# Performance work log

Hardware: AMD Instinct MI355X
Metric: run time of the kernel (lower is better)

## Reference

```python
import jax, jax.numpy as jnp
import numpy as np

N, D_IN, D_OUT, E = 8192, 2048, 2048, 8


def setup_inputs() -> dict:
    key = jax.random.key(0)
    k0, k1, k2, k3, k4, k5 = jax.random.split(key, 6)
    s = 1.0 / np.sqrt(D_IN)  # torch nn.Linear default init range
    return {
        "inputs": jax.random.normal(k0, (N, D_IN), jnp.float32),
        "condition": jax.random.normal(k1, (N, D_IN), jnp.float32),
        "Wp": jax.random.uniform(k2, (E, D_IN), jnp.float32, -s, s),
        "bp": jax.random.uniform(k3, (E,), jnp.float32, -s, s),
        "We": jax.random.uniform(k4, (E, D_OUT, D_IN), jnp.float32, -s, s),
        "be": jax.random.uniform(k5, (E, D_OUT), jnp.float32, -s, s),
    }


def reference(inputs, condition, Wp, bp, We, be):
    # predictor: gating logits [N, E]
    prediction = condition @ Wp.T + bp
    # straight-through multiplier: value == 1, gradient flows to prediction
    multiply = jnp.ones_like(prediction) + (prediction - jax.lax.stop_gradient(prediction))
    # run ALL experts on the full batch (faithful to the original): [E, N, F]
    expert_out = jnp.einsum('nd,efd->enf', inputs, We) + be[:, None, :]
    combined = multiply.T[:, :, None] * expert_out  # [E, N, F]
    # select the argmax expert per row
    idx = jnp.argmax(prediction, axis=-1)  # [N]
    result = combined[idx, jnp.arange(prediction.shape[0])]  # [N, F]
    return result
```

## Files before the change

### kernel.cpp

```cpp
#include <hip/hip_runtime.h>
#include <hip/hip_bf16.h>
#include <stdint.h>

#define N_ROWS 8192
#define DIN 2048
#define DOUT 2048
#define NE 8

#define BM 128
#define BN 128
#define BK 64
#define MAX_RT 71

typedef __bf16 bf16x8 __attribute__((ext_vector_type(8)));
typedef float f32x4 __attribute__((ext_vector_type(4)));

__device__ __forceinline__ uint32_t f2bf(float f) {
  uint32_t u = __builtin_bit_cast(uint32_t, f);
  uint32_t r = u + 0x7FFFu + ((u >> 16) & 1u);
  return r >> 16;
}

__device__ __forceinline__ void gl2lds16(const void* g, void* l) {
  __builtin_amdgcn_global_load_lds(
      (const __attribute__((address_space(1))) unsigned int*)g,
      (__attribute__((address_space(3))) unsigned int*)l, 16, 0, 0);
}

__global__ __launch_bounds__(256) void gate_kernel(
    const float* __restrict__ cond, const float* __restrict__ Wp,
    const float* __restrict__ bp, int* __restrict__ idx)
{
  const int lane = threadIdx.x & 63;
  const int wid  = threadIdx.x >> 6;
  const int row  = blockIdx.x * 4 + wid;

  double acc[NE];
  #pragma unroll
  for (int e = 0; e < NE; ++e) acc[e] = 0.0;

  const float4* crow = (const float4*)(cond + (size_t)row * DIN);
  const float4* wp4  = (const float4*)Wp;
  #pragma unroll
  for (int i = 0; i < DIN / 256; ++i) {
    float4 c = crow[i * 64 + lane];
    #pragma unroll
    for (int e = 0; e < NE; ++e) {
      float4 w = wp4[e * (DIN / 4) + i * 64 + lane];
      acc[e] += (double)c.x * w.x + (double)c.y * w.y
              + (double)c.z * w.z + (double)c.w * w.w;
    }
  }
  #pragma unroll
  for (int e = 0; e < NE; ++e) {
    double v = acc[e];
    #pragma unroll
    for (int off = 32; off > 0; off >>= 1) v += __shfl_down(v, off, 64);
    acc[e] = v;
  }
  if (lane == 0) {
    int best = 0; double bv = acc[0] + (double)bp[0];
    #pragma unroll
    for (int e = 1; e < NE; ++e) {
      double v = acc[e] + (double)bp[e];
      if (v > bv) { bv = v; best = e; }
    }
    idx[row] = best;
  }
}

__global__ __launch_bounds__(256) void hist_kernel(
    const int* __restrict__ idx, int* __restrict__ counts)
{
  __shared__ int lc[NE];
  const int t = threadIdx.x;
  if (t < NE) lc[t] = 0;
  __syncthreads();
  int n = blockIdx.x * 256 + t;
  atomicAdd(&lc[idx[n]], 1);
  __syncthreads();
  if (t < NE && lc[t] > 0) atomicAdd(&counts[t], lc[t]);
}

__global__ void scan_kernel(const int* __restrict__ counts, int* __restrict__ offsets) {
  if (threadIdx.x == 0 && blockIdx.x == 0) {
    int s = 0;
    for (int e = 0; e < NE; ++e) { offsets[e] = s; s += counts[e]; }
  }
}

__global__ __launch_bounds__(256) void scatter_kernel(
    const int* __restrict__ idx, const int* __restrict__ offsets,
    int* __restrict__ fill, int* __restrict__ rows)
{
  __shared__ int lc[NE], lb[NE];
  const int t = threadIdx.x;
  if (t < NE) lc[t] = 0;
  __syncthreads();
  int n = blockIdx.x * 256 + t;
  int e = idx[n];
  int my = atomicAdd(&lc[e], 1);
  __syncthreads();
  if (t < NE) lb[t] = (lc[t] > 0) ? atomicAdd(&fill[t], lc[t]) : 0;
  __syncthreads();
  rows[offsets[e] + lb[e] + my] = n;
}

__global__ __launch_bounds__(256) void conv_kernel(
    const float* __restrict__ src, __hip_bfloat16* __restrict__ dst, size_t nchunks)
{
  const size_t stride = (size_t)gridDim.x * 256;
  for (size_t c = (size_t)blockIdx.x * 256 + threadIdx.x; c < nchunks; c += stride) {
    float4 v0 = ((const float4*)src)[c * 2];
    float4 v1 = ((const float4*)src)[c * 2 + 1];
    uint4 o;
    o.x = f2bf(v0.x) | (f2bf(v0.y) << 16);
    o.y = f2bf(v0.z) | (f2bf(v0.w) << 16);
    o.z = f2bf(v1.x) | (f2bf(v1.y) << 16);
    o.w = f2bf(v1.z) | (f2bf(v1.w) << 16);
    ((uint4*)dst)[c] = o;
  }
}

__global__ __launch_bounds__(256) void moe_gemm3(
    const __hip_bfloat16* __restrict__ Xb, const __hip_bfloat16* __restrict__ Web,
    const float* __restrict__ be, const int* __restrict__ counts,
    const int* __restrict__ offsets, const int* __restrict__ rows,
    float* __restrict__ out)
{
  __shared__ __align__(16) __hip_bfloat16 As[2][BM * BK];
  __shared__ __align__(16) __hip_bfloat16 Bs[2][BN * BK];
  __shared__ int rowid[BM];

  const int ct = blockIdx.x;
  const int rt = blockIdx.y;

  int e = 0, racc = 0, cnt = 0;
  for (; e < NE; ++e) {
    cnt = counts[e];
    int tiles = (cnt + BM - 1) / BM;
    if (rt < racc + tiles) break;
    racc += tiles;
  }
  if (e == NE) return;
  const int row0 = (rt - racc) * BM;
  const int base = offsets[e];
  const int t = threadIdx.x;

  if (t < BM)
    rowid[t] = (row0 + t < cnt) ? rows[base + row0 + t] : -1;
  __syncthreads();

  const __hip_bfloat16* aSrcP[4];
  #pragma unroll
  for (int p = 0; p < 4; ++p) {
    int c = p * 256 + t;
    int gr = rowid[c >> 3];
    if (gr < 0) gr = 0;
    aSrcP[p] = Xb + (size_t)gr * DIN + (c & 7) * 8;
  }
  const size_t bcol0 = (size_t)e * DOUT + (size_t)ct * BN;
  const __hip_bfloat16* bSrc0 = Web + (bcol0 + (t >> 3)) * DIN + (t & 7) * 8;

  const int lane = t & 63;
  const int wv   = t >> 6;
  const int wr   = wv >> 1, wc = wv & 1;
  const int g    = lane >> 4, fr = lane & 15;

  f32x4 acc[4][4];
  #pragma unroll
  for (int m = 0; m < 4; ++m)
    #pragma unroll
    for (int n = 0; n < 4; ++n)
      acc[m][n] = 0.0f;

#define STAGE(buf, k0) do {                                                     \
    _Pragma("unroll")                                                           \
    for (int p = 0; p < 4; ++p) {                                               \
      gl2lds16(aSrcP[p] + (k0), (char*)As[buf] + p * 4096 + t * 16);            \
      gl2lds16(bSrc0 + (size_t)p * 32 * DIN + (k0),                             \
               (char*)Bs[buf] + p * 4096 + t * 16);                             \
    } } while (0)

#define COMPUTE(buf) do {                                                       \
    _Pragma("unroll")                                                           \
    for (int kk = 0; kk < BK; kk += 32) {                                       \
      bf16x8 av[4], bv[4];                                                      \
      _Pragma("unroll")                                                         \
      for (int m = 0; m < 4; ++m)                                               \
        av[m] = *(const bf16x8*)((const char*)As[buf] +                         \
                 (wr * 64 + m * 16 + fr) * (BK * 2) + (kk + g * 8) * 2);        \
      _Pragma("unroll")                                                         \
      for (int n = 0; n < 4; ++n)                                               \
        bv[n] = *(const bf16x8*)((const char*)Bs[buf] +                         \
                 (wc * 64 + n * 16 + fr) * (BK * 2) + (kk + g * 8) * 2);        \
      __builtin_amdgcn_s_setprio(1);                                            \
      _Pragma("unroll")                                                         \
      for (int m = 0; m < 4; ++m)                                               \
        _Pragma("unroll")                                                       \
        for (int n = 0; n < 4; ++n)                                             \
          acc[m][n] = __builtin_amdgcn_mfma_f32_16x16x32_bf16(av[m], bv[n],     \
                                                              acc[m][n], 0,0,0);\
      __builtin_amdgcn_s_setprio(0);                                            \
    } } while (0)

  STAGE(0, 0);
  __syncthreads();
  int k0 = BK;
  #pragma unroll 1
  for (int it = 0; it < 15; ++it) {
    STAGE(1, k0); COMPUTE(0); __syncthreads(); k0 += BK;
    STAGE(0, k0); COMPUTE(1); __syncthreads(); k0 += BK;
  }
  STAGE(1, k0); COMPUTE(0); __syncthreads();
  COMPUTE(1);

#undef STAGE
#undef COMPUTE

  const float* berow = be + (size_t)e * DOUT + (size_t)ct * BN + wc * 64;
  #pragma unroll
  for (int m = 0; m < 4; ++m) {
    #pragma unroll
    for (int j = 0; j < 4; ++j) {
      int r = wr * 64 + m * 16 + g * 4 + j;
      int grow = rowid[r];
      if (grow < 0) continue;
      float* orow = out + (size_t)grow * DOUT + (size_t)ct * BN + wc * 64;
      #pragma unroll
      for (int n = 0; n < 4; ++n)
        orow[n * 16 + fr] = acc[m][n][j] + berow[n * 16 + fr];
    }
  }
}

__global__ __launch_bounds__(256) void moe_gemm_fb(
    const float* __restrict__ X, const float* __restrict__ We,
    const float* __restrict__ be, const int* __restrict__ counts,
    const int* __restrict__ offsets, const int* __restrict__ rows,
    float* __restrict__ out)
{
  __shared__ __align__(16) unsigned char Asb[BM * BK * 2];
  __shared__ __align__(16) unsigned char Bsb[BN * BK * 2];
  __shared__ int rowid[BM];

  const int ct = blockIdx.x;
  const int rt = blockIdx.y;

  int e = 0, racc = 0, cnt = 0;
  for (; e < NE; ++e) {
    cnt = counts[e];
    int tiles = (cnt + BM - 1) / BM;
    if (rt < racc + tiles) break;
    racc += tiles;
  }
  if (e == NE) return;
  const int row0 = (rt - racc) * BM;
  const int base = offsets[e];

  if (threadIdx.x < BM) {
    int r = row0 + threadIdx.x;
    rowid[threadIdx.x] = (r < cnt) ? rows[base + r] : -1;
  }
  __syncthreads();

  const int t    = threadIdx.x;
  const int lane = t & 63;
  const int wv   = t >> 6;
  const int wr   = wv >> 1, wc = wv & 1;
  const int g    = lane >> 4, fr = lane & 15;
  const int srow = t >> 4;
  const int skq  = t & 15;

  f32x4 acc[4][4];
  #pragma unroll
  for (int m = 0; m < 4; ++m)
    #pragma unroll
    for (int n = 0; n < 4; ++n)
      acc[m][n] = 0.0f;

  const size_t bcol0 = (size_t)e * DOUT + (size_t)ct * BN;

  for (int k0 = 0; k0 < DIN; k0 += BK) {
    #pragma unroll
    for (int p = 0; p < 8; ++p) {
      int r = p * 16 + srow;
      int gr = rowid[r];
      float4 v = make_float4(0.f, 0.f, 0.f, 0.f);
      if (gr >= 0)
        v = *(const float4*)(X + (size_t)gr * DIN + k0 + skq * 4);
      uint32_t w0 = f2bf(v.x) | (f2bf(v.y) << 16);
      uint32_t w1 = f2bf(v.z) | (f2bf(v.w) << 16);
      int byte = r * (BK * 2) + ((skq * 8) ^ ((r & 7) << 4));
      *(uint2*)(Asb + byte) = make_uint2(w0, w1);
    }
    #pragma unroll
    for (int p = 0; p < 8; ++p) {
      int r = p * 16 + srow;
      float4 v = *(const float4*)(We + (bcol0 + r) * DIN + k0 + skq * 4);
      uint32_t w0 = f2bf(v.x) | (f2bf(v.y) << 16);
      uint32_t w1 = f2bf(v.z) | (f2bf(v.w) << 16);
      int byte = r * (BK * 2) + ((skq * 8) ^ ((r & 7) << 4));
      *(uint2*)(Bsb + byte) = make_uint2(w0, w1);
    }
    __syncthreads();

    #pragma unroll
    for (int kk = 0; kk < BK; kk += 32) {
      bf16x8 av[4], bv[4];
      #pragma unroll
      for (int m = 0; m < 4; ++m) {
        int r = wr * 64 + m * 16 + fr;
        int byte = r * (BK * 2) + ((((kk + g * 8) * 2)) ^ ((r & 7) << 4));
        av[m] = *(const bf16x8*)(Asb + byte);
      }
      #pragma unroll
      for (int n = 0; n < 4; ++n) {
        int c = wc * 64 + n * 16 + fr;
        int byte = c * (BK * 2) + ((((kk + g * 8) * 2)) ^ ((c & 7) << 4));
        bv[n] = *(const bf16x8*)(Bsb + byte);
      }
      #pragma unroll
      for (int m = 0; m < 4; ++m)
        #pragma unroll
        for (int n = 0; n < 4; ++n)
          acc[m][n] = __builtin_amdgcn_mfma_f32_16x16x32_bf16(av[m], bv[n], acc[m][n], 0, 0, 0);
    }
    __syncthreads();
  }

  const float* berow = be + (size_t)e * DOUT + (size_t)ct * BN + wc * 64;
  #pragma unroll
  for (int m = 0; m < 4; ++m) {
    #pragma unroll
    for (int j = 0; j < 4; ++j) {
      int r = wr * 64 + m * 16 + g * 4 + j;
      int grow = rowid[r];
      if (grow < 0) continue;
      float* orow = out + (size_t)grow * DOUT + (size_t)ct * BN + wc * 64;
      #pragma unroll
      for (int n = 0; n < 4; ++n)
        orow[n * 16 + fr] = acc[m][n][j] + berow[n * 16 + fr];
    }
  }
}

extern "C" void kernel_launch(void* const* d_in, const int* in_sizes, int n_in,
                              void* d_out, int out_size, void* d_ws, size_t ws_size,
                              hipStream_t stream) {
  const float* X    = (const float*)d_in[0];
  const float* cond = (const float*)d_in[1];
  const float* Wp   = (const float*)d_in[2];
  const float* bp   = (const float*)d_in[3];
  const float* We   = (const float*)d_in[4];
  const float* be   = (const float*)d_in[5];
  float* out = (float*)d_out;

  int* counts  = (int*)d_ws;
  int* offsets = counts + 8;
  int* fill    = counts + 16;
  int* idx     = (int*)((char*)d_ws + 256);
  int* rows    = idx + N_ROWS;
  const size_t XB_OFF  = 65792;
  const size_t WEB_OFF = XB_OFF + (size_t)N_ROWS * DIN * 2;
  const size_t WS_NEED = WEB_OFF + (size_t)NE * DOUT * DIN * 2;

  hipMemsetAsync(d_ws, 0, 256, stream);
  gate_kernel<<<N_ROWS / 4, 256, 0, stream>>>(cond, Wp, bp, idx);
  hist_kernel<<<N_ROWS / 256, 256, 0, stream>>>(idx, counts);
  scan_kernel<<<1, 64, 0, stream>>>(counts, offsets);
  scatter_kernel<<<N_ROWS / 256, 256, 0, stream>>>(idx, offsets, fill, rows);

  if (ws_size >= WS_NEED) {
    __hip_bfloat16* Xb  = (__hip_bfloat16*)((char*)d_ws + XB_OFF);
    __hip_bfloat16* Web = (__hip_bfloat16*)((char*)d_ws + WEB_OFF);
    conv_kernel<<<2048, 256, 0, stream>>>(X, Xb, (size_t)N_ROWS * DIN / 8);
    conv_kernel<<<2048, 256, 0, stream>>>(We, Web, (size_t)NE * DOUT * DIN / 8);
    moe_gemm3<<<dim3(DOUT / BN, MAX_RT), 256, 0, stream>>>(Xb, Web, be, counts, offsets, rows, out);
  } else {
    moe_gemm_fb<<<dim3(DOUT / BN, MAX_RT), 256, 0, stream>>>(X, We, be, counts, offsets, rows, out);
  }
}
```

Before: 225.9 us.

## Replace grouped MoE GEMM with 256x256 tile, 8-wave, swizzled LDS, phased pipeline

Replaces the 128x128, 4-wave expert GEMM with a 256x256 tile kernel using 512 threads. It splits each tile into four 128x128 quadrant phases, uses XOR-swizzled LDS to avoid bank conflicts, and tracks prefetch with explicit vmcnt waits. A 1D grid is remapped so that blocks sharing a row tile run close together. The aim is more data reuse per loaded byte and better MFMA utilisation, at the cost of fewer blocks (occupancy 1) and more tail waste from 256-row padding per expert.

```diff
diff --git a/kernel.cpp b/kernel.cpp
--- a/kernel.cpp
+++ b/kernel.cpp
@@ -6,6 +6,12 @@
 #define DIN 2048
 #define DOUT 2048
 #define NE 8
+
+#define BM2 256
+#define BN2 256
+#define BK2 64
+#define RT2 39
+#define NBLK2 (8 * RT2)
 
 #define BM 128
 #define BN 128
@@ -122,116 +128,173 @@
   }
 }
 
-__global__ __launch_bounds__(256) void moe_gemm3(
+__global__ __launch_bounds__(512, 1) void moe_gemm8(
     const __hip_bfloat16* __restrict__ Xb, const __hip_bfloat16* __restrict__ Web,
     const float* __restrict__ be, const int* __restrict__ counts,
-    const int* __restrict__ offsets, const int* __restrict__ rows,
-    float* __restrict__ out)
-{
-  __shared__ __align__(16) __hip_bfloat16 As[2][BM * BK];
-  __shared__ __align__(16) __hip_bfloat16 Bs[2][BN * BK];
-  __shared__ int rowid[BM];
-
-  const int ct = blockIdx.x;
-  const int rt = blockIdx.y;
-
-  int e = 0, racc = 0, cnt = 0;
+    const int* __restrict__ rows, float* __restrict__ out)
+{
+  __shared__ __align__(16) __hip_bfloat16 Asm[2][2][128 * 64];
+  __shared__ __align__(16) __hip_bfloat16 Bsm[2][2][128 * 64];
+  __shared__ int rowid[256];
+
+  const int bid = blockIdx.x;
+  const int w = (bid & 7) * RT2 + (bid >> 3);
+  const int ct = w / RT2;
+  const int rt = w % RT2;
+
+  int e = 0, racc = 0, cnt = 0, base = 0;
   for (; e < NE; ++e) {
     cnt = counts[e];
-    int tiles = (cnt + BM - 1) / BM;
+    int tiles = (cnt + BM2 - 1) / BM2;
     if (rt < racc + tiles) break;
-    racc += tiles;
+    racc += tiles; base += cnt;
   }
   if (e == NE) return;
-  const int row0 = (rt - racc) * BM;
-  const int base = offsets[e];
-  const int t = threadIdx.x;
-
-  if (t < BM)
-    rowid[t] = (row0 + t < cnt) ? rows[base + row0 + t] : -1;
-  __syncthreads();
-
-  const __hip_bfloat16* aSrcP[4];
-  #pragma unroll
-  for (int p = 0; p < 4; ++p) {
-    int c = p * 256 + t;
-    int gr = rowid[c >> 3];
-    if (gr < 0) gr = 0;
-    aSrcP[p] = Xb + (size_t)gr * DIN + (c & 7) * 8;
-  }
-  const size_t bcol0 = (size_t)e * DOUT + (size_t)ct * BN;
-  const __hip_bfloat16* bSrc0 = Web + (bcol0 + (t >> 3)) * DIN + (t & 7) * 8;
-
-  const int lane = t & 63;
-  const int wv   = t >> 6;
-  const int wr   = wv >> 1, wc = wv & 1;
-  const int g    = lane >> 4, fr = lane & 15;
-
-  f32x4 acc[4][4];
-  #pragma unroll
-  for (int m = 0; m < 4; ++m)
-    #pragma unroll
-    for (int n = 0; n < 4; ++n)
-      acc[m][n] = 0.0f;
-
-#define STAGE(buf, k0) do {                                                     \
-    _Pragma("unroll")                                                           \
-    for (int p = 0; p < 4; ++p) {                                               \
-      gl2lds16(aSrcP[p] + (k0), (char*)As[buf] + p * 4096 + t * 16);            \
-      gl2lds16(bSrc0 + (size_t)p * 32 * DIN + (k0),                             \
-               (char*)Bs[buf] + p * 4096 + t * 16);                             \
-    } } while (0)
-
-#define COMPUTE(buf) do {                                                       \
-    _Pragma("unroll")                                                           \
-    for (int kk = 0; kk < BK; kk += 32) {                                       \
-      bf16x8 av[4], bv[4];                                                      \
-      _Pragma("unroll")                                                         \
-      for (int m = 0; m < 4; ++m)                                               \
-        av[m] = *(const bf16x8*)((const char*)As[buf] +                         \
-                 (wr * 64 + m * 16 + fr) * (BK * 2) + (kk + g * 8) * 2);        \
-      _Pragma("unroll")                                                         \
-      for (int n = 0; n < 4; ++n)                                               \
-        bv[n] = *(const bf16x8*)((const char*)Bs[buf] +                         \
-                 (wc * 64 + n * 16 + fr) * (BK * 2) + (kk + g * 8) * 2);        \
-      __builtin_amdgcn_s_setprio(1);                                            \
-      _Pragma("unroll")                                                         \
-      for (int m = 0; m < 4; ++m)                                               \
-        _Pragma("unroll")                                                       \
-        for (int n = 0; n < 4; ++n)                                             \
-          acc[m][n] = __builtin_amdgcn_mfma_f32_16x16x32_bf16(av[m], bv[n],     \
-                                                              acc[m][n], 0,0,0);\
-      __builtin_amdgcn_s_setprio(0);                                            \
-    } } while (0)
-
-  STAGE(0, 0);
-  __syncthreads();
-  int k0 = BK;
+  const int row0 = (rt - racc) * BM2;
+  const int tid = threadIdx.x;
+  if (tid < 256)
+    rowid[tid] = (row0 + tid < cnt) ? rows[base + row0 + tid] : -1;
+  __syncthreads();
+
+  const int d0 = tid * 16;
+  const __hip_bfloat16 *aP[2][2], *bP[2][2];
+  #pragma unroll
+  for (int p = 0; p < 2; ++p) {
+    int d = p * 8192 + d0;
+    int sd = d ^ (((d >> 9) & 1) << 5);
+    int r128 = sd >> 7;
+    int cel = (sd & 127) >> 1;
+    #pragma unroll
+    for (int h = 0; h < 2; ++h) {
+      int gr = rowid[h * 128 + r128];
+      if (gr < 0) gr = 0;
+      aP[h][p] = Xb + (size_t)gr * DIN + cel;
+      bP[h][p] = Web + ((size_t)e * DOUT + ct * BN2 + h * 128 + r128) * DIN + cel;
+    }
+  }
+
+  const int lane = tid & 63, wid = tid >> 6;
+  const int wm = wid >> 2, wn = wid & 3;
+  const int g = lane >> 4, fr = lane & 15;
+  const int arh = wm * 64 + fr;
+  const int brh = wn * 32 + fr;
+
+  f32x4 acc[2][2][4][2];
+  #pragma unroll
+  for (int a = 0; a < 2; ++a)
+    #pragma unroll
+    for (int b = 0; b < 2; ++b)
+      #pragma unroll
+      for (int m = 0; m < 4; ++m)
+        #pragma unroll
+        for (int n = 0; n < 2; ++n)
+          acc[a][b][m][n] = 0.0f;
+
+  bf16x8 av[2][4], bv[2][2];
+
+#define STG_A(buf, h, kel) do {                                              \
+    gl2lds16(aP[h][0] + (kel), (char*)&Asm[buf][h][0] + d0);                 \
+    gl2lds16(aP[h][1] + (kel), (char*)&Asm[buf][h][0] + 8192 + d0); } while (0)
+#define STG_B(buf, h, kel) do {                                              \
+    gl2lds16(bP[h][0] + (kel), (char*)&Bsm[buf][h][0] + d0);                 \
+    gl2lds16(bP[h][1] + (kel), (char*)&Bsm[buf][h][0] + 8192 + d0); } while (0)
+
+#define READ_A(c, h) do { const char* Ab_ = (const char*)&Asm[c][h][0];      \
+    _Pragma("unroll") for (int kk = 0; kk < 2; ++kk)                         \
+    _Pragma("unroll") for (int mi = 0; mi < 4; ++mi) {                       \
+      int rh = arh + mi * 16;                                                \
+      int by = (rh * 128 + kk * 64 + g * 16) ^ (((rh >> 2) & 1) << 5);       \
+      av[kk][mi] = *(const bf16x8*)(Ab_ + by); } } while (0)
+
+#define READ_B(c, h) do { const char* Bb_ = (const char*)&Bsm[c][h][0];      \
+    _Pragma("unroll") for (int kk = 0; kk < 2; ++kk)                         \
+    _Pragma("unroll") for (int ni = 0; ni < 2; ++ni) {                       \
+      int rh = brh + ni * 16;                                                \
+      int by = (rh * 128 + kk * 64 + g * 16) ^ (((rh >> 2) & 1) << 5);       \
+      bv[kk][ni] = *(const bf16x8*)(Bb_ + by); } } while (0)
+
+#define LGKM0 do { asm volatile("s_waitcnt lgkmcnt(0)" ::: "memory");        \
+                   __builtin_amdgcn_sched_barrier(0); } while (0)
+#define VMC4  do { asm volatile("s_waitcnt vmcnt(4)" ::: "memory");          \
+                   __builtin_amdgcn_sched_barrier(0); } while (0)
+#define VMC0  do { asm volatile("s_waitcnt vmcnt(0)" ::: "memory");          \
+                   __builtin_amdgcn_sched_barrier(0); } while (0)
+
+#define MFMA_PH(mh, nh) do { __builtin_amdgcn_s_setprio(1);                  \
+    _Pragma("unroll") for (int kk = 0; kk < 2; ++kk)                         \
+    _Pragma("unroll") for (int mi = 0; mi < 4; ++mi)                         \
+    _Pragma("unroll") for (int ni = 0; ni < 2; ++ni)                         \
+      acc[mh][nh][mi][ni] = __builtin_amdgcn_mfma_f32_16x16x32_bf16(         \
+          av[kk][mi], bv[kk][ni], acc[mh][nh][mi][ni], 0, 0, 0);             \
+    __builtin_amdgcn_s_setprio(0); } while (0)
+
+  STG_A(0, 0, 0);  STG_B(0, 0, 0);  STG_A(0, 1, 0);  STG_B(0, 1, 0);
+  STG_A(1, 0, 64); STG_B(1, 0, 64);
+  VMC4;
+  __syncthreads();
+
+  const int T = DIN / BK2;
   #pragma unroll 1
-  for (int it = 0; it < 15; ++it) {
-    STAGE(1, k0); COMPUTE(0); __syncthreads(); k0 += BK;
-    STAGE(0, k0); COMPUTE(1); __syncthreads(); k0 += BK;
-  }
-  STAGE(1, k0); COMPUTE(0); __syncthreads();
-  COMPUTE(1);
-
-#undef STAGE
-#undef COMPUTE
-
-  const float* berow = be + (size_t)e * DOUT + (size_t)ct * BN + wc * 64;
-  #pragma unroll
-  for (int m = 0; m < 4; ++m) {
-    #pragma unroll
-    for (int j = 0; j < 4; ++j) {
-      int r = wr * 64 + m * 16 + g * 4 + j;
-      int grow = rowid[r];
-      if (grow < 0) continue;
-      float* orow = out + (size_t)grow * DOUT + (size_t)ct * BN + wc * 64;
-      #pragma unroll
-      for (int n = 0; n < 4; ++n)
-        orow[n * 16 + fr] = acc[m][n][j] + berow[n * 16 + fr];
-    }
-  }
+  for (int t = 0; t < T; ++t) {
+    const int c = t & 1, o = c ^ 1;
+    const int k1 = (t + 1) * BK2, k2 = (t + 2) * BK2;
+    const bool s1 = (t + 1 < T), s2 = (t + 2 < T);
+
+    READ_A(c, 0); READ_B(c, 0);
+    if (s1) STG_A(o, 1, k1);
+    __syncthreads(); LGKM0;
+    MFMA_PH(0, 0);
+    __syncthreads();
+
+    READ_B(c, 1);
+    if (s1) STG_B(o, 1, k1);
+    __syncthreads(); LGKM0;
+    MFMA_PH(0, 1);
+    __syncthreads();
+
+    READ_A(c, 1); READ_B(c, 0);
+    if (s2) STG_A(c, 0, k2);
+    __syncthreads(); LGKM0;
+    MFMA_PH(1, 0);
+    __syncthreads();
+
+    READ_B(c, 1);
+    if (s2) STG_B(c, 0, k2);
+    __syncthreads(); LGKM0;
+    MFMA_PH(1, 1);
+    if (s2) { VMC4; } else { VMC0; }
+    __syncthreads();
+  }
+
+#undef STG_A
+#undef STG_B
+#undef READ_A
+#undef READ_B
+#undef MFMA_PH
+
+  float beh[2][2];
+  #pragma unroll
+  for (int nh = 0; nh < 2; ++nh)
+    #pragma unroll
+    for (int ni = 0; ni < 2; ++ni)
+      beh[nh][ni] = be[(size_t)e * DOUT + ct * BN2 + nh * 128 + wn * 32 + ni * 16 + fr];
+
+  #pragma unroll
+  for (int mh = 0; mh < 2; ++mh)
+    #pragma unroll
+    for (int mi = 0; mi < 4; ++mi)
+      #pragma unroll
+      for (int j = 0; j < 4; ++j) {
+        int R = mh * 128 + wm * 64 + mi * 16 + g * 4 + j;
+        int grow = rowid[R];
+        if (grow < 0) continue;
+        float* orow = out + (size_t)grow * DOUT + ct * BN2;
+        #pragma unroll
+        for (int nh = 0; nh < 2; ++nh)
+          #pragma unroll
+          for (int ni = 0; ni < 2; ++ni)
+            orow[nh * 128 + wn * 32 + ni * 16 + fr] = acc[mh][nh][mi][ni][j] + beh[nh][ni];
+      }
 }
 
 __global__ __launch_bounds__(256) void moe_gemm_fb(
@@ -376,7 +439,7 @@
     __hip_bfloat16* Web = (__hip_bfloat16*)((char*)d_ws + WEB_OFF);
     conv_kernel<<<2048, 256, 0, stream>>>(X, Xb, (size_t)N_ROWS * DIN / 8);
     conv_kernel<<<2048, 256, 0, stream>>>(We, Web, (size_t)NE * DOUT * DIN / 8);
-    moe_gemm3<<<dim3(DOUT / BN, MAX_RT), 256, 0, stream>>>(Xb, Web, be, counts, offsets, rows, out);
+    moe_gemm8<<<NBLK2, 512, 0, stream>>>(Xb, Web, be, counts, rows, out);
   } else {
     moe_gemm_fb<<<dim3(DOUT / BN, MAX_RT), 256, 0, stream>>>(X, We, be, counts, offsets, rows, out);
   }
```

After: 305.8 us. +35.4%, slower.
